# Kernel optimization log

Measured on AMD Instinct MI355X. Metric: run time of the kernel, lower is better.

The kernel has to match this reference:

```python
import jax, jax.numpy as jnp
import numpy as np
import math

D_MODEL = 1024
N_HEAD = 16
D_HEAD = D_MODEL // N_HEAD
B, T = 4, 2048


def setup_inputs() -> dict:
    key = jax.random.key(0)
    ks = jax.random.split(key, 9)
    x = jax.random.normal(ks[0], (B, T, D_MODEL), dtype=jnp.float32)
    # causal mask, broadcastable to [B, H, T, T]; mask==0 -> -1e9
    mask = jnp.tril(jnp.ones((T, T), dtype=bool))[None, None, :, :]
    # Xavier-uniform linear weights (stored as [in, out] for x @ W), zero biases
    limit = math.sqrt(6.0 / (D_MODEL + D_MODEL))
    def w(k):
        return jax.random.uniform(k, (D_MODEL, D_MODEL), dtype=jnp.float32, minval=-limit, maxval=limit)
    return {
        "x": x,
        "mask": mask,
        "wq": w(ks[1]), "bq": jnp.zeros((D_MODEL,), jnp.float32),
        "wk": w(ks[2]), "bk": jnp.zeros((D_MODEL,), jnp.float32),
        "wv": w(ks[3]), "bv": jnp.zeros((D_MODEL,), jnp.float32),
        "wo": w(ks[4]), "bo": jnp.zeros((D_MODEL,), jnp.float32),
    }


def reference(x, mask, wq, bq, wk, bk, wv, bv, wo, bo):
    b, t, c = x.shape
    h, dh = N_HEAD, D_HEAD
    # [B,T,C] -> [B,H,T,dh]
    def heads(y):
        return y.reshape(b, t, h, dh).transpose(0, 2, 1, 3)
    q = heads(x @ wq + bq)
    k = heads(x @ wk + bk)
    v = heads(x @ wv + bv)
    att = jnp.einsum("bhqd,bhkd->bhqk", q, k) / math.sqrt(dh)
    att = jnp.where(mask, att, jnp.float32(-1e9))
    att = jax.nn.softmax(att, axis=-1)  # dropout is identity in eval mode
    out = jnp.einsum("bhqk,bhkd->bhqd", att, v)
    out = out.transpose(0, 2, 1, 3).reshape(b, t, c)
    return out @ wo + bo
```

## Files before the change

### kernel.cpp

```cpp
#include <hip/hip_runtime.h>

typedef __bf16 bf16_t;
typedef bf16_t bf16x8 __attribute__((ext_vector_type(8)));
typedef bf16_t bf16x4 __attribute__((ext_vector_type(4)));
typedef float  f32x4  __attribute__((ext_vector_type(4)));
typedef float  f32x16 __attribute__((ext_vector_type(16)));
typedef unsigned int u32;
typedef u32 u32x2 __attribute__((ext_vector_type(2)));
typedef u32 u32x4 __attribute__((ext_vector_type(4)));

#define T_SEQ 2048
#define C_DIM 1024
#define NH    16
#define DH    64
#define BATCH 4
#define M_TOK (BATCH * T_SEQ)

#define Q_SCALE 0.1803368801111137f
#define DEFER_THR 8.0f

#define AS1 __attribute__((address_space(1)))
#define AS3 __attribute__((address_space(3)))

__device__ __forceinline__ void gld_lds16(const bf16_t* g, bf16_t* l) {
  __builtin_amdgcn_global_load_lds(
      (const AS1 u32*)(uintptr_t)g,
      (AS3 u32*)(u32)(uintptr_t)l, 16, 0, 0);
}

__device__ __forceinline__ void plswap(u32& a, u32& b) {
  u32x2 r = __builtin_amdgcn_permlane32_swap(a, b, false, false);
  a = r[0]; b = r[1];
}
__device__ __forceinline__ float xmax32(float x) {
  u32 a = __builtin_bit_cast(u32, x), b = a;
  plswap(a, b);
  return fmaxf(__builtin_bit_cast(float, a), __builtin_bit_cast(float, b));
}
__device__ __forceinline__ float xsum32(float x) {
  u32 a = __builtin_bit_cast(u32, x), b = a;
  plswap(a, b);
  return __builtin_bit_cast(float, a) + __builtin_bit_cast(float, b);
}

__device__ __forceinline__ u32 pack_bf16_pair(float v0, float v1) {
  const unsigned short b0 = __builtin_bit_cast(unsigned short, (bf16_t)v0);
  const unsigned short b1 = __builtin_bit_cast(unsigned short, (bf16_t)v1);
  return ((u32)b1 << 16) | (u32)b0;
}

__global__ __launch_bounds__(256) void msa_cvt_x(const float* __restrict__ x,
                                                 bf16_t* __restrict__ xb, int n4) {
  int i = blockIdx.x * 256 + threadIdx.x;
  if (i < n4) {
    const float4 v = ((const float4*)x)[i];
    bf16x4 o;
    o[0] = (bf16_t)v.x; o[1] = (bf16_t)v.y; o[2] = (bf16_t)v.z; o[3] = (bf16_t)v.w;
    ((bf16x4*)xb)[i] = o;
  }
}

__global__ __launch_bounds__(256) void msa_transpose_w(
    const float* __restrict__ wq, const float* __restrict__ wk,
    const float* __restrict__ wv, const float* __restrict__ wo,
    bf16_t* __restrict__ wt_qkv, bf16_t* __restrict__ wt_o) {
  __shared__ float tile[32][33];
  const int a = blockIdx.z;
  const float* src = (a == 0) ? wq : (a == 1) ? wk : (a == 2) ? wv : wo;
  bf16_t* dst = (a < 3) ? (wt_qkv + (size_t)a * C_DIM * C_DIM) : wt_o;
  const int tx = threadIdx.x & 31, ty = threadIdx.x >> 5;
  const int bi = blockIdx.y * 32, bj = blockIdx.x * 32;
#pragma unroll
  for (int p = 0; p < 4; p++) {
    int r = p * 8 + ty;
    tile[r][tx] = src[(size_t)(bi + r) * C_DIM + bj + tx];
  }
  __syncthreads();
#pragma unroll
  for (int p = 0; p < 4; p++) {
    int r = p * 8 + ty;
    dst[(size_t)(bj + r) * C_DIM + bi + tx] = (bf16_t)tile[tx][r];
  }
}

#define GQ_BUF 16384

#define GEMM_CORE(APTR, BPTR, NT)                                              \
  __shared__ __align__(16) char lds[3 * GQ_BUF];                               \
  const int tid = threadIdx.x;                                                 \
  const int w = tid >> 6, lane = tid & 63;                                     \
  const int lr = lane & 15, lg = lane >> 4;                                    \
  int bx_, by_;                                                                \
  {                                                                            \
    const int gx = gridDim.x;                                                  \
    const int nwg = gx * gridDim.y;                                            \
    int lin = blockIdx.y * gx + blockIdx.x;                                    \
    lin = (lin & 7) * (nwg >> 3) + (lin >> 3);                                 \
    bx_ = lin % gx; by_ = lin / gx;                                            \
  }                                                                            \
  const int m0 = by_ * 128;                                                    \
  const int n0 = bx_ * 128;                                                    \
  const int wm = (w >> 1) * 64, wn = (w & 1) * 64;                             \
  const int rsw = (lg * 16) ^ ((lr & 3) << 4);                                 \
  int Aoff[4], Boff[4];                                                        \
  _Pragma("unroll") for (int f = 0; f < 4; f++) {                              \
    Aoff[f] = (wm + f * 16 + lr) * 64 + rsw;                                   \
    Boff[f] = 8192 + (wn + f * 16 + lr) * 64 + rsw;                            \
  }                                                                            \
  const int idx0 = tid, idx1 = 256 + tid;                                      \
  const int r0 = idx0 >> 2, c0_ = ((idx0 & 3) ^ (r0 & 3)) * 8;                 \
  const int r1 = idx1 >> 2, c1_ = ((idx1 & 3) ^ (r1 & 3)) * 8;                 \
  const bf16_t* gA0 = (APTR) + (size_t)(m0 + r0) * C_DIM + c0_;                \
  const bf16_t* gA1 = (APTR) + (size_t)(m0 + r1) * C_DIM + c1_;                \
  const bf16_t* gB0 = (BPTR) + (size_t)(n0 + r0) * C_DIM + c0_;                \
  const bf16_t* gB1 = (BPTR) + (size_t)(n0 + r1) * C_DIM + c1_;                \
  f32x4 acc[4][4];                                                             \
  _Pragma("unroll") for (int i = 0; i < 4; i++)                                \
    _Pragma("unroll") for (int j = 0; j < 4; j++)                              \
      acc[i][j] = (f32x4){0.f, 0.f, 0.f, 0.f};                                 \
  GSTG(0, 0);                                                                  \
  GSTG(1, GQ_BUF);                                                             \
  asm volatile("s_waitcnt vmcnt(4)" ::: "memory");                             \
  __builtin_amdgcn_s_barrier();                                                \
  __builtin_amdgcn_sched_barrier(0);                                           \
  int cb = 0;                                                                  \
  for (int kt = 0; kt < (NT); ++kt) {                                          \
    const char* base = lds + cb * GQ_BUF;                                      \
    bf16x8 a[4], b[4];                                                         \
    _Pragma("unroll") for (int f = 0; f < 4; f++) {                            \
      a[f] = *(const bf16x8*)(base + Aoff[f]);                                 \
      b[f] = *(const bf16x8*)(base + Boff[f]);                                 \
    }                                                                          \
    if (kt < (NT)-2) {                                                         \
      int sb = cb + 2; if (sb >= 3) sb -= 3;                                   \
      GSTG(kt + 2, sb * GQ_BUF);                                               \
    }                                                                          \
    __builtin_amdgcn_s_setprio(1);                                             \
    _Pragma("unroll") for (int mf = 0; mf < 4; mf++)                           \
      _Pragma("unroll") for (int nf = 0; nf < 4; nf++)                         \
        acc[mf][nf] = __builtin_amdgcn_mfma_f32_16x16x32_bf16(                 \
            a[mf], b[nf], acc[mf][nf], 0, 0, 0);                               \
    __builtin_amdgcn_s_setprio(0);                                             \
    if (kt < (NT)-2) {                                                         \
      asm volatile("s_waitcnt vmcnt(4)" ::: "memory");                         \
    } else {                                                                   \
      asm volatile("s_waitcnt vmcnt(0)" ::: "memory");                         \
    }                                                                          \
    __builtin_amdgcn_s_barrier();                                              \
    __builtin_amdgcn_sched_barrier(0);                                         \
    if (++cb == 3) cb = 0;                                                     \
  }

#define GSTG(KT, BB)                                                           \
  {                                                                            \
    bf16_t* d_ = (bf16_t*)(lds + (BB));                                        \
    gld_lds16(gA0 + (KT) * 32, d_ + tid * 8);                                  \
    gld_lds16(gA1 + (KT) * 32, d_ + 2048 + tid * 8);                           \
    gld_lds16(gB0 + (KT) * 32, d_ + 4096 + tid * 8);                           \
    gld_lds16(gB1 + (KT) * 32, d_ + 6144 + tid * 8);                           \
  }

__global__ __launch_bounds__(256, 3) void msa_gemm_qkv(
    const bf16_t* __restrict__ xb, const bf16_t* __restrict__ wt,
    const float* __restrict__ bq, const float* __restrict__ bk,
    const float* __restrict__ bv,
    bf16_t* __restrict__ qo, bf16_t* __restrict__ ko, bf16_t* __restrict__ vto) {
  GEMM_CORE(xb, wt, 32)

  const int g = n0 >> 10;
  if (g == 2) {
#pragma unroll
    for (int nb = 0; nb < 4; nb++) {
      const int c = ((n0 + wn) & 1023) + nb * 16 + lr;
      const int h = c >> 6, d = c & 63;
      const float bias = bv[c];
      bf16_t* vrow = vto + (((size_t)((m0 >> 11) * NH + h)) * DH + d) * T_SEQ;
#pragma unroll
      for (int mb = 0; mb < 4; mb++) {
        const int t = (m0 & 2047) + wm + mb * 16 + lg * 4;
        u32x2 pr;
        pr[0] = pack_bf16_pair(acc[mb][nb][0] + bias, acc[mb][nb][1] + bias);
        pr[1] = pack_bf16_pair(acc[mb][nb][2] + bias, acc[mb][nb][3] + bias);
        *reinterpret_cast<u32x2*>(vrow + t) = pr;
      }
    }
  } else {
#pragma unroll
    for (int nb = 0; nb < 4; nb++) {
      const int n = n0 + wn + nb * 16 + lr;
      const int c = n & 1023, h = c >> 6, d = c & 63;
      const float bias = (g == 0) ? bq[c] : bk[c];
#pragma unroll
      for (int mb = 0; mb < 4; mb++) {
#pragma unroll
        for (int r = 0; r < 4; r++) {
          const int m = m0 + wm + mb * 16 + lg * 4 + r;
          const int bi = m >> 11, t = m & (T_SEQ - 1);
          float v = acc[mb][nb][r] + bias;
          if (g == 0)
            qo[(((size_t)bi * NH + h) * T_SEQ + t) * DH + d] = (bf16_t)(v * Q_SCALE);
          else
            ko[(((size_t)bi * NH + h) * T_SEQ + t) * DH + d] = (bf16_t)v;
        }
      }
    }
  }
}

__global__ __launch_bounds__(256, 3) void msa_gemm_out(
    const bf16_t* __restrict__ ab, const bf16_t* __restrict__ wt,
    const float* __restrict__ bo, float* __restrict__ out) {
  GEMM_CORE(ab, wt, 32)

#pragma unroll
  for (int nb = 0; nb < 4; nb++) {
    const int n = n0 + wn + nb * 16 + lr;
    const float bias = bo[n];
#pragma unroll
    for (int mb = 0; mb < 4; mb++) {
#pragma unroll
      for (int r = 0; r < 4; r++) {
        const int m = m0 + wm + mb * 16 + lg * 4 + r;
        out[(size_t)m * C_DIM + n] = acc[mb][nb][r] + bias;
      }
    }
  }
}

__device__ __forceinline__ void pack_frag(const f32x16& s, bf16x8& pa0, bf16x8& pa1) {
  u32 pk8[8];
#pragma unroll
  for (int i = 0; i < 8; i++) pk8[i] = pack_bf16_pair(s[2 * i], s[2 * i + 1]);
  u32 f0w0 = pk8[0], f0w2 = pk8[2];
  u32 f0w1 = pk8[1], f0w3 = pk8[3];
  u32 f1w0 = pk8[4], f1w2 = pk8[6];
  u32 f1w1 = pk8[5], f1w3 = pk8[7];
  plswap(f0w0, f0w2);
  plswap(f0w1, f0w3);
  plswap(f1w0, f1w2);
  plswap(f1w1, f1w3);
  const u32x4 q0v = {f0w0, f0w1, f0w2, f0w3};
  const u32x4 q1v = {f1w0, f1w1, f1w2, f1w3};
  pa0 = __builtin_bit_cast(bf16x8, q0v);
  pa1 = __builtin_bit_cast(bf16x8, q1v);
}

__device__ __forceinline__ void sm_pack(f32x16& s, float& m_run, float& l_run,
                                        f32x16& o0, f32x16& o1,
                                        bf16x8& pa0, bf16x8& pa1) {
  float t0 = fmaxf(fmaxf(s[0], s[1]), s[2]);
  float t1 = fmaxf(fmaxf(s[3], s[4]), s[5]);
  float t2 = fmaxf(fmaxf(s[6], s[7]), s[8]);
  float t3 = fmaxf(fmaxf(s[9], s[10]), s[11]);
  float t4 = fmaxf(fmaxf(s[12], s[13]), s[14]);
  float t5 = fmaxf(fmaxf(t0, t1), s[15]);
  float mt = fmaxf(fmaxf(fmaxf(t2, t3), t4), t5);
  mt = xmax32(mt);

  if (__any(mt > m_run + DEFER_THR)) {
    const float mnew = fmaxf(m_run, mt);
    const float al = __builtin_amdgcn_exp2f(m_run - mnew);
    m_run = mnew;
    l_run *= al;
#pragma unroll
    for (int r = 0; r < 16; r++) { o0[r] *= al; o1[r] *= al; }
  }

#pragma unroll
  for (int r = 0; r < 16; r++) s[r] = __builtin_amdgcn_exp2f(s[r] - m_run);
  {
    float a0 = (s[0] + s[1]) + (s[2] + s[3]);
    float a1 = (s[4] + s[5]) + (s[6] + s[7]);
    float a2 = (s[8] + s[9]) + (s[10] + s[11]);
    float a3 = (s[12] + s[13]) + (s[14] + s[15]);
    l_run += xsum32((a0 + a1) + (a2 + a3));
  }
  pack_frag(s, pa0, pa1);
}

__device__ __forceinline__ void store_o(f32x16& o0, f32x16& o1, float l_fin,
                                        bf16_t* __restrict__ orow, const int hi) {
  const float inv = 1.0f / l_fin;
#pragma unroll
  for (int db = 0; db < 2; db++) {
#pragma unroll
    for (int r = 0; r < 16; r += 2) {
      const int d = db * 32 + (r & 3) + 8 * (r >> 2) + 4 * hi;
      const float v0 = (db ? o1[r] : o0[r]) * inv;
      const float v1 = (db ? o1[r + 1] : o0[r + 1]) * inv;
      *reinterpret_cast<u32*>(orow + d) = pack_bf16_pair(v0, v1);
    }
  }
}

__global__ __launch_bounds__(256, 2) void msa_attn_lds(
    const bf16_t* __restrict__ Q, const bf16_t* __restrict__ K,
    const bf16_t* __restrict__ Vt, bf16_t* __restrict__ O) {
  __shared__ __align__(16) char lds[16384];
  const int tid = threadIdx.x;
  const int w = tid >> 6;
  const int lane = tid & 63;
  const int l31 = lane & 31;
  const int hi = lane >> 5;
  const int bh = blockIdx.x;
  const int pg = blockIdx.y;
  const int p = pg * 4 + w;
  const int tS = p, tL = 63 - p;
  const int q0S = tS * 32, q0L = tL * 32;
  const int KT_MAX = 63 - 4 * pg;

  const bf16_t* Qh = Q + (size_t)bh * T_SEQ * DH;
  const bf16_t* Kh = K + (size_t)bh * T_SEQ * DH;
  const bf16_t* Vh = Vt + (size_t)bh * DH * T_SEQ;

  bf16x8 qfL[4], qfS[4];
#pragma unroll
  for (int dc = 0; dc < 4; dc++) {
    qfL[dc] = *(const bf16x8*)(Qh + (size_t)(q0L + l31) * DH + dc * 16 + hi * 8);
    qfS[dc] = *(const bf16x8*)(Qh + (size_t)(q0S + l31) * DH + dc * 16 + hi * 8);
  }

  f32x16 oL0, oL1, oS0, oS1;
#pragma unroll
  for (int r = 0; r < 16; r++) { oL0[r] = 0.f; oL1[r] = 0.f; oS0[r] = 0.f; oS1[r] = 0.f; }
  float mL = -1e30f, lL = 0.f, mS = -1e30f, lS = 0.f;
  const f32x16 z16 = {};

  const int ksw = (l31 & 7) << 4;
  const int vsw = (l31 & 3) << 4;
  const int krow = tid >> 3;
  const int kce = ((16 * (tid & 7)) ^ ((krow & 7) << 4)) >> 1;
  const int vrow = tid >> 2;
  const int vce = ((16 * (tid & 3)) ^ ((vrow & 3) << 4)) >> 1;

#define STAGE(KT, BUF)                                                         \
  {                                                                            \
    const int jj = (KT) * 32;                                                  \
    bf16_t* base_ = (bf16_t*)(lds + (BUF) * 8192);                             \
    gld_lds16(Kh + (size_t)(jj + krow) * DH + kce, base_ + tid * 8);           \
    gld_lds16(Vh + (size_t)vrow * T_SEQ + jj + vce, base_ + 2048 + tid * 8);   \
  }

  STAGE(0, 0);
  __syncthreads();

  for (int kt = 0; kt <= KT_MAX; ++kt) {
    const int buf = kt & 1;
    if (kt < KT_MAX) STAGE(kt + 1, buf ^ 1);

    const bool doL = (kt <= tL);
    if (doL) {
      const char* kb = lds + buf * 8192;
      const char* vb = kb + 4096;
      bf16x8 kf[4];
#pragma unroll
      for (int dc = 0; dc < 4; dc++)
        kf[dc] = *(const bf16x8*)(kb + l31 * 128 + ((dc * 32 + hi * 16) ^ ksw));
      const bf16x8 vf00 = *(const bf16x8*)(vb + l31 * 64 + ((hi * 16) ^ vsw));
      const bf16x8 vf01 = *(const bf16x8*)(vb + l31 * 64 + ((32 + hi * 16) ^ vsw));
      const bf16x8 vf10 = *(const bf16x8*)(vb + (32 + l31) * 64 + ((hi * 16) ^ vsw));
      const bf16x8 vf11 = *(const bf16x8*)(vb + (32 + l31) * 64 + ((32 + hi * 16) ^ vsw));

      const bool doS = (kt <= tS);
      f32x16 sL = __builtin_amdgcn_mfma_f32_32x32x16_bf16(kf[0], qfL[0], z16, 0, 0, 0);
#pragma unroll
      for (int dc = 1; dc < 4; dc++)
        sL = __builtin_amdgcn_mfma_f32_32x32x16_bf16(kf[dc], qfL[dc], sL, 0, 0, 0);
      f32x16 sS;
      if (doS) {
        sS = __builtin_amdgcn_mfma_f32_32x32x16_bf16(kf[0], qfS[0], z16, 0, 0, 0);
#pragma unroll
        for (int dc = 1; dc < 4; dc++)
          sS = __builtin_amdgcn_mfma_f32_32x32x16_bf16(kf[dc], qfS[dc], sS, 0, 0, 0);
      }
      if (kt == tL) {
#pragma unroll
        for (int r = 0; r < 16; r++) {
          const int jrow = (r & 3) + 8 * (r >> 2) + 4 * hi;
          if (jrow > l31) sL[r] = -1e30f;
        }
      }
      if (kt == tS) {
#pragma unroll
        for (int r = 0; r < 16; r++) {
          const int jrow = (r & 3) + 8 * (r >> 2) + 4 * hi;
          if (jrow > l31) sS[r] = -1e30f;
        }
      }
      bf16x8 paL0, paL1;
      sm_pack(sL, mL, lL, oL0, oL1, paL0, paL1);
      oL0 = __builtin_amdgcn_mfma_f32_32x32x16_bf16(vf00, paL0, oL0, 0, 0, 0);
      oL1 = __builtin_amdgcn_mfma_f32_32x32x16_bf16(vf10, paL0, oL1, 0, 0, 0);
      oL0 = __builtin_amdgcn_mfma_f32_32x32x16_bf16(vf01, paL1, oL0, 0, 0, 0);
      oL1 = __builtin_amdgcn_mfma_f32_32x32x16_bf16(vf11, paL1, oL1, 0, 0, 0);
      if (doS) {
        bf16x8 paS0, paS1;
        sm_pack(sS, mS, lS, oS0, oS1, paS0, paS1);
        oS0 = __builtin_amdgcn_mfma_f32_32x32x16_bf16(vf00, paS0, oS0, 0, 0, 0);
        oS1 = __builtin_amdgcn_mfma_f32_32x32x16_bf16(vf10, paS0, oS1, 0, 0, 0);
        oS0 = __builtin_amdgcn_mfma_f32_32x32x16_bf16(vf01, paS1, oS0, 0, 0, 0);
        oS1 = __builtin_amdgcn_mfma_f32_32x32x16_bf16(vf11, paS1, oS1, 0, 0, 0);
      }
    }
    __syncthreads();
  }
#undef STAGE

  const int b = bh >> 4, h = bh & 15;
  store_o(oL0, oL1, lL, O + ((size_t)b * T_SEQ + q0L + l31) * C_DIM + h * DH, hi);
  store_o(oS0, oS1, lS, O + ((size_t)b * T_SEQ + q0S + l31) * C_DIM + h * DH, hi);
}

extern "C" void kernel_launch(void* const* d_in, const int* in_sizes, int n_in,
                              void* d_out, int out_size, void* d_ws, size_t ws_size,
                              hipStream_t stream) {
  const float* x  = (const float*)d_in[0];
  const float* wq = (const float*)d_in[2];
  const float* bq = (const float*)d_in[3];
  const float* wk = (const float*)d_in[4];
  const float* bk = (const float*)d_in[5];
  const float* wv = (const float*)d_in[6];
  const float* bv = (const float*)d_in[7];
  const float* wo = (const float*)d_in[8];
  const float* bo = (const float*)d_in[9];

  char* ws = (char*)d_ws;
  bf16_t* xb     = (bf16_t*)(ws);
  bf16_t* wt_qkv = (bf16_t*)(ws + (16ull << 20));
  bf16_t* wt_o   = (bf16_t*)(ws + (22ull << 20));
  bf16_t* qb     = (bf16_t*)(ws + (24ull << 20));
  bf16_t* kb     = (bf16_t*)(ws + (40ull << 20));
  bf16_t* vtb    = (bf16_t*)(ws + (56ull << 20));
  bf16_t* attn_o = xb;

  const int n4 = M_TOK * C_DIM / 4;
  msa_cvt_x<<<n4 / 256, 256, 0, stream>>>(x, xb, n4);
  msa_transpose_w<<<dim3(32, 32, 4), 256, 0, stream>>>(wq, wk, wv, wo, wt_qkv, wt_o);
  msa_gemm_qkv<<<dim3(24, 64), 256, 0, stream>>>(xb, wt_qkv, bq, bk, bv, qb, kb, vtb);
  msa_attn_lds<<<dim3(64, 8), 256, 0, stream>>>(qb, kb, vtb, attn_o);
  msa_gemm_out<<<dim3(8, 64), 256, 0, stream>>>(attn_o, wt_o, bo, (float*)d_out);
}
```

Measured before the change: 169.4 us.

## Triple-buffer attention K/V staging and drop GEMM block swizzle

Result: no change. 169.7 us (+0.2%).

```diff
diff --git a/kernel.cpp b/kernel.cpp
--- a/kernel.cpp
+++ b/kernel.cpp
@@ -90,16 +90,8 @@
   const int tid = threadIdx.x;                                                 \
   const int w = tid >> 6, lane = tid & 63;                                     \
   const int lr = lane & 15, lg = lane >> 4;                                    \
-  int bx_, by_;                                                                \
-  {                                                                            \
-    const int gx = gridDim.x;                                                  \
-    const int nwg = gx * gridDim.y;                                            \
-    int lin = blockIdx.y * gx + blockIdx.x;                                    \
-    lin = (lin & 7) * (nwg >> 3) + (lin >> 3);                                 \
-    bx_ = lin % gx; by_ = lin / gx;                                            \
-  }                                                                            \
-  const int m0 = by_ * 128;                                                    \
-  const int n0 = bx_ * 128;                                                    \
+  const int m0 = blockIdx.y * 128;                                             \
+  const int n0 = blockIdx.x * 128;                                             \
   const int wm = (w >> 1) * 64, wn = (w & 1) * 64;                             \
   const int rsw = (lg * 16) ^ ((lr & 3) << 4);                                 \
   int Aoff[4], Boff[4];                                                        \
@@ -296,7 +288,7 @@
 __global__ __launch_bounds__(256, 2) void msa_attn_lds(
     const bf16_t* __restrict__ Q, const bf16_t* __restrict__ K,
     const bf16_t* __restrict__ Vt, bf16_t* __restrict__ O) {
-  __shared__ __align__(16) char lds[16384];
+  __shared__ __align__(16) char lds[3 * 8192];
   const int tid = threadIdx.x;
   const int w = tid >> 6;
   const int lane = tid & 63;
@@ -342,15 +334,21 @@
   }
 
   STAGE(0, 0);
-  __syncthreads();
-
+  STAGE(1, 1);
+  asm volatile("s_waitcnt vmcnt(2)" ::: "memory");
+  __builtin_amdgcn_s_barrier();
+  __builtin_amdgcn_sched_barrier(0);
+
+  int cb = 0;
   for (int kt = 0; kt <= KT_MAX; ++kt) {
-    const int buf = kt & 1;
-    if (kt < KT_MAX) STAGE(kt + 1, buf ^ 1);
+    if (kt + 2 <= KT_MAX) {
+      int sb = cb + 2; if (sb >= 3) sb -= 3;
+      STAGE(kt + 2, sb);
+    }
 
     const bool doL = (kt <= tL);
     if (doL) {
-      const char* kb = lds + buf * 8192;
+      const char* kb = lds + cb * 8192;
       const char* vb = kb + 4096;
       bf16x8 kf[4];
 #pragma unroll
@@ -402,7 +400,15 @@
         oS1 = __builtin_amdgcn_mfma_f32_32x32x16_bf16(vf11, paS1, oS1, 0, 0, 0);
       }
     }
-    __syncthreads();
+
+    if (kt < KT_MAX - 1) {
+      asm volatile("s_waitcnt vmcnt(2)" ::: "memory");
+    } else {
+      asm volatile("s_waitcnt vmcnt(0)" ::: "memory");
+    }
+    __builtin_amdgcn_s_barrier();
+    __builtin_amdgcn_sched_barrier(0);
+    if (++cb == 3) cb = 0;
   }
 #undef STAGE
 
```
